# Optimization experiments

Hardware: AMD Instinct MI355X
Metric: run time of the kernel (lower is better)

## Reference

```python
import jax, jax.numpy as jnp
import numpy as np

DIST_MULT = 0.1
CLIP_LOW = 0.0
EPS = 1e-6


def setup_inputs() -> dict:
    key = jax.random.key(0)
    k1, _ = jax.random.split(key)
    x_msg_binned = jax.random.normal(k1, (8, 64, 512, 16), dtype=jnp.float32)
    msk = jnp.ones((8, 64, 512, 1), dtype=jnp.float32)
    return {"x_msg_binned": x_msg_binned, "msk": msk}


def reference(x_msg_binned, msk):
    # A: (B, bins, N, F) masked node features
    A = x_msg_binned * msk
    na = jnp.sum(A * A, axis=-1)  # (B, bins, N)
    # Gram matrix: (B, bins, N, N)
    G = jnp.einsum("bknf,bkmf->bknm", A, A)
    D = jnp.sqrt(jnp.maximum(na[..., :, None] - 2.0 * G + na[..., None, :], EPS))
    dm = jnp.exp(-DIST_MULT * D)[..., None]  # (B, bins, N, N, 1)
    return jnp.clip(dm, CLIP_LOW, 1.0)
```

## Files before the change

kernel.cpp:

```cpp
#include <hip/hip_runtime.h>


typedef float    f32x4 __attribute__((ext_vector_type(4)));
typedef _Float16 f16x4 __attribute__((ext_vector_type(4)));

#define NEG_DIST_LOG2E (-0.14426950408889634f)
#define EPS_F 1e-6f

__global__ __launch_bounds__(256) void node_pair_gaussian_kernel(
    const float* __restrict__ x,
    const float* __restrict__ msk,
    float* __restrict__ out)
{
    __shared__ __align__(16) _Float16 lds_n[128][20];
    __shared__ __align__(16) _Float16 lds_m[128][20];
    __shared__ __align__(16) float na_n[128];
    __shared__ __align__(16) float na_m[128];

    const int tid   = threadIdx.x;
    const int tile  = blockIdx.x;
    const int slice = blockIdx.y;
    const int n0 = (tile >> 2) << 7;
    const int m0 = (tile & 3) << 7;

    const float* xs = x   + (size_t)slice * (512 * 16);
    const float* ms = msk + (size_t)slice * 512;

    #pragma unroll
    for (int it = 0; it < 2; ++it) {
        const int task = tid + it * 256;
        const int node = task & 127;
        const int f4   = task >> 7;
        {
            const f32x4 v = *(const f32x4*)(xs + (size_t)(n0 + node) * 16 + f4 * 4);
            const float mm = ms[n0 + node];
            f16x4 h = { (_Float16)(v.x * mm), (_Float16)(v.y * mm),
                        (_Float16)(v.z * mm), (_Float16)(v.w * mm) };
            *(f16x4*)&lds_n[node][f4 * 4] = h;
        }
        {
            const f32x4 v = *(const f32x4*)(xs + (size_t)(m0 + node) * 16 + f4 * 4);
            const float mm = ms[m0 + node];
            f16x4 h = { (_Float16)(v.x * mm), (_Float16)(v.y * mm),
                        (_Float16)(v.z * mm), (_Float16)(v.w * mm) };
            *(f16x4*)&lds_m[node][f4 * 4] = h;
        }
    }
    __syncthreads();

    {
        const int node = tid & 127;
        const _Float16* p = (tid < 128) ? &lds_m[node][0] : &lds_n[node][0];
        float s = 0.0f;
        #pragma unroll
        for (int f4 = 0; f4 < 4; ++f4) {
            const f16x4 h = *(const f16x4*)&p[f4 * 4];
            const float a0 = (float)h.x, a1 = (float)h.y;
            const float a2 = (float)h.z, a3 = (float)h.w;
            s = fmaf(a0, a0, s); s = fmaf(a1, a1, s);
            s = fmaf(a2, a2, s); s = fmaf(a3, a3, s);
        }
        if (tid < 128) na_m[node] = s; else na_n[node] = s;
    }
    __syncthreads();

    const int lane = tid & 63;
    const int wv   = tid >> 6;
    const int lr   = lane & 15;
    const int q    = lane >> 4;
    const int mb   = wv * 32;

    f16x4 afr[2];
    #pragma unroll
    for (int a = 0; a < 2; ++a)
        afr[a] = *(const f16x4*)&lds_m[mb + a * 16 + lr][q * 4];
    f16x4 bfr[8];
    #pragma unroll
    for (int b = 0; b < 8; ++b)
        bfr[b] = *(const f16x4*)&lds_n[b * 16 + lr][q * 4];

    f32x4 acc[8][2];
    #pragma unroll
    for (int b = 0; b < 8; ++b)
        #pragma unroll
        for (int a = 0; a < 2; ++a) {
            f32x4 z = {0.0f, 0.0f, 0.0f, 0.0f};
            acc[b][a] = __builtin_amdgcn_mfma_f32_16x16x16f16(afr[a], bfr[b], z, 0, 0, 0);
        }

    f32x4 nm[2];
    nm[0] = *(const f32x4*)&na_m[mb + q * 4];
    nm[1] = *(const f32x4*)&na_m[mb + 16 + q * 4];

    float* outs = out + (size_t)slice * (512 * 512) + (size_t)n0 * 512 + (m0 + mb);

    #pragma unroll
    for (int b = 0; b < 8; ++b) {
        const float nn = na_n[b * 16 + lr];
        const size_t rowoff = (size_t)(b * 16 + lr) * 512;
        #pragma unroll
        for (int a = 0; a < 2; ++a) {
            f32x4 r;
            #pragma unroll
            for (int j = 0; j < 4; ++j) {
                float s = fmaf(-2.0f, acc[b][a][j], nn + nm[a][j]);
                s = fmaxf(s, EPS_F);
                const float d = __builtin_amdgcn_sqrtf(s);
                const float e = __builtin_amdgcn_exp2f(d * NEG_DIST_LOG2E);
                r[j] = fminf(e, 1.0f);
            }
            __builtin_nontemporal_store(r, (f32x4*)(outs + rowoff + a * 16 + q * 4));
        }
    }
}

extern "C" void kernel_launch(void* const* d_in, const int* in_sizes, int n_in,
                              void* d_out, int out_size, void* d_ws, size_t ws_size,
                              hipStream_t stream) {
    const float* x   = (const float*)d_in[0];
    const float* msk = (const float*)d_in[1];
    float* out = (float*)d_out;

    dim3 grid(16, 512);
    node_pair_gaussian_kernel<<<grid, 256, 0, stream>>>(x, msk, out);
}
```

Baseline: 601.4 us.

## Switch Gram tile to 32x32x16 MFMA with per-row scalar stores

Replaces the sixteen 16x16x16 MFMAs per wave with four 32x32x16 f16 MFMAs covering 32 columns by 128 rows, loading 8-wide f16 fragments from LDS rows padded to 24 halves. The epilogue now writes one scalar per lane per output row, so each wave row-store covers 32 contiguous floats, replacing the earlier 16-byte vector nontemporal stores. This is meant to cut MFMA issue count and fragment loads. The cost is narrower, regular (not nontemporal) stores on a kernel that is write-bound, plus more LDS reads of na_n per element.

Result: faster. 544.4 us (-9.5%).

```diff
diff --git a/kernel.cpp b/kernel.cpp
--- a/kernel.cpp
+++ b/kernel.cpp
@@ -1,19 +1,22 @@
 #include <hip/hip_runtime.h>
 
 
-typedef float    f32x4 __attribute__((ext_vector_type(4)));
-typedef _Float16 f16x4 __attribute__((ext_vector_type(4)));
+typedef float    f32x4  __attribute__((ext_vector_type(4)));
+typedef float    f32x16 __attribute__((ext_vector_type(16)));
+typedef _Float16 f16x4  __attribute__((ext_vector_type(4)));
+typedef _Float16 f16x8  __attribute__((ext_vector_type(8)));
 
 #define NEG_DIST_LOG2E (-0.14426950408889634f)
 #define EPS_F 1e-6f
+#define LROW 24
 
 __global__ __launch_bounds__(256) void node_pair_gaussian_kernel(
     const float* __restrict__ x,
     const float* __restrict__ msk,
     float* __restrict__ out)
 {
-    __shared__ __align__(16) _Float16 lds_n[128][20];
-    __shared__ __align__(16) _Float16 lds_m[128][20];
+    __shared__ __align__(16) _Float16 lds_n[128][LROW];
+    __shared__ __align__(16) _Float16 lds_m[128][LROW];
     __shared__ __align__(16) float na_n[128];
     __shared__ __align__(16) float na_m[128];
 
@@ -65,51 +68,32 @@
     __syncthreads();
 
     const int lane = tid & 63;
-    const int wv   = tid >> 6;
-    const int lr   = lane & 15;
-    const int q    = lane >> 4;
-    const int mb   = wv * 32;
+    const int w    = tid >> 6;
+    const int jl   = lane & 31;
+    const int h    = lane >> 5;
 
-    f16x4 afr[2];
-    #pragma unroll
-    for (int a = 0; a < 2; ++a)
-        afr[a] = *(const f16x4*)&lds_m[mb + a * 16 + lr][q * 4];
-    f16x4 bfr[8];
-    #pragma unroll
-    for (int b = 0; b < 8; ++b)
-        bfr[b] = *(const f16x4*)&lds_n[b * 16 + lr][q * 4];
+    const f16x8 bfr = *(const f16x8*)&lds_m[w * 32 + jl][h * 8];
+    const float nm  = na_m[w * 32 + jl];
 
-    f32x4 acc[8][2];
-    #pragma unroll
-    for (int b = 0; b < 8; ++b)
-        #pragma unroll
-        for (int a = 0; a < 2; ++a) {
-            f32x4 z = {0.0f, 0.0f, 0.0f, 0.0f};
-            acc[b][a] = __builtin_amdgcn_mfma_f32_16x16x16f16(afr[a], bfr[b], z, 0, 0, 0);
-        }
-
-    f32x4 nm[2];
-    nm[0] = *(const f32x4*)&na_m[mb + q * 4];
-    nm[1] = *(const f32x4*)&na_m[mb + 16 + q * 4];
-
-    float* outs = out + (size_t)slice * (512 * 512) + (size_t)n0 * 512 + (m0 + mb);
+    float* const outs = out + (size_t)slice * (512 * 512)
+                            + (size_t)n0 * 512 + (m0 + w * 32);
 
     #pragma unroll
-    for (int b = 0; b < 8; ++b) {
-        const float nn = na_n[b * 16 + lr];
-        const size_t rowoff = (size_t)(b * 16 + lr) * 512;
+    for (int rt = 0; rt < 4; ++rt) {
+        const f16x8 afr = *(const f16x8*)&lds_n[rt * 32 + jl][h * 8];
+        const f32x16 z = {0.0f,0.0f,0.0f,0.0f, 0.0f,0.0f,0.0f,0.0f,
+                          0.0f,0.0f,0.0f,0.0f, 0.0f,0.0f,0.0f,0.0f};
+        const f32x16 acc = __builtin_amdgcn_mfma_f32_32x32x16_f16(afr, bfr, z, 0, 0, 0);
+
         #pragma unroll
-        for (int a = 0; a < 2; ++a) {
-            f32x4 r;
-            #pragma unroll
-            for (int j = 0; j < 4; ++j) {
-                float s = fmaf(-2.0f, acc[b][a][j], nn + nm[a][j]);
-                s = fmaxf(s, EPS_F);
-                const float d = __builtin_amdgcn_sqrtf(s);
-                const float e = __builtin_amdgcn_exp2f(d * NEG_DIST_LOG2E);
-                r[j] = fminf(e, 1.0f);
-            }
-            __builtin_nontemporal_store(r, (f32x4*)(outs + rowoff + a * 16 + q * 4));
+        for (int r = 0; r < 16; ++r) {
+            const int row = rt * 32 + 4 * h + (r & 3) + 8 * (r >> 2);
+            const float nn = na_n[row];
+            float s = fmaf(-2.0f, acc[r], nn + nm);
+            s = fmaxf(s, EPS_F);
+            const float d = __builtin_amdgcn_sqrtf(s);
+            const float e = __builtin_amdgcn_exp2f(d * NEG_DIST_LOG2E);
+            outs[(size_t)row * 512 + jl] = fminf(e, 1.0f);
         }
     }
 }
```
